# Performance work log

Hardware: AMD Instinct MI355X
Metric: run time of the kernel (lower is better)

## Reference

```python
import jax, jax.numpy as jnp
import numpy as np

H = 8
D_MODEL = 512
D_K = D_MODEL // H
NEG = -1e9


def setup_inputs() -> dict:
    key = jax.random.key(0)
    ks = jax.random.split(key, 12)
    N, Lq, Lk = 2, 4096, 4096
    inp = {
        "query": jax.random.normal(ks[0], (N, Lq, D_MODEL), dtype=jnp.float32),
        "key": jax.random.normal(ks[1], (N, Lk, D_MODEL), dtype=jnp.float32),
        "value": jax.random.normal(ks[2], (N, Lk, D_MODEL), dtype=jnp.float32),
        "mask": jnp.ones((N, 1, Lk), dtype=jnp.int32),
    }
    scale = 0.02
    for i, nm in enumerate(["q", "k", "v", "o"]):
        inp[f"W{nm}"] = scale * jax.random.normal(ks[3 + i], (D_MODEL, D_MODEL), dtype=jnp.float32)
        inp[f"b{nm}"] = jnp.zeros((D_MODEL,), dtype=jnp.float32)
    return inp


def reference(query, key, value, mask, Wq, bq, Wk, bk, Wv, bv, Wo, bo):
    # torch Linear: y = x @ W.T + b
    N, Lq, _ = query.shape
    Lk = key.shape[1]
    q = (query @ Wq.T + bq).reshape(N, Lq, H, D_K)   # (N,Lq,h,dk)
    k = (key @ Wk.T + bk).reshape(N, Lk, H, D_K)     # (N,Lk,h,dk)
    v = (value @ Wv.T + bv).reshape(N, Lk, H, D_K)   # (N,Lk,h,dk)
    # scores: (N,h,Lq,Lk)
    scores = jnp.einsum("bqhd,bkhd->bhqk", q, k) / jnp.sqrt(jnp.float32(D_K))
    # mask (N,1,Lk) or (N,Lq,Lk) -> broadcast over heads (and Lq if singleton)
    m = mask[:, None, :, :]  # (N,1,1|Lq,Lk)
    scores = jnp.where(m == 0, jnp.float32(NEG), scores)
    attn = jax.nn.softmax(scores, axis=-1)
    # dropout is identity in eval mode (deterministic reference)
    out = jnp.einsum("bhqk,bkhd->bqhd", attn, v).reshape(N, Lq, D_MODEL)
    return out @ Wo.T + bo
```

## Files before the change

### kernel.cpp

```cpp
#include <hip/hip_runtime.h>
#include <hip/hip_bf16.h>

#define H 8
#define DM 512
#define DK 64
#define LSEQ 4096
#define NB 2
#define NSPLIT 2
#define KSPAN (LSEQ / NSPLIT)
#define NIT (KSPAN / 64)

#define QSCALE 0.18033688011112042f

typedef float f32x4 __attribute__((ext_vector_type(4)));
typedef __bf16 bf16x8 __attribute__((ext_vector_type(8)));
typedef __bf16 bf16x2 __attribute__((ext_vector_type(2)));
typedef unsigned short u16;

__device__ __forceinline__ u16 f2bf(float f) {
    union { float f; unsigned u; } v{f};
    return (u16)((v.u + 0x8000u) >> 16);
}

__device__ __forceinline__ unsigned pkbf(float a, float b) {
#if __has_builtin(__builtin_amdgcn_cvt_pk_bf16_f32)
    union { bf16x2 v; unsigned u; } x;
    x.v = __builtin_amdgcn_cvt_pk_bf16_f32(a, b);
    return x.u;
#else
    union { float f; unsigned u; } x{a}, y{b};
    return ((x.u + 0x8000u) >> 16) | ((y.u + 0x8000u) & 0xffff0000u);
#endif
}

__device__ __forceinline__ ushort4 cvt4(float4 a) {
    union { ushort4 s; uint2 u; } o;
    o.u.x = pkbf(a.x, a.y);
    o.u.y = pkbf(a.z, a.w);
    return o.s;
}

__device__ __forceinline__ float2 ubf2(unsigned u) {
    union { float f; unsigned v; } a, b;
    a.v = u << 16;
    b.v = u & 0xffff0000u;
    return make_float2(a.f, b.f);
}

__device__ __forceinline__ float fexp2(float x) {
#if __has_builtin(__builtin_amdgcn_exp2f)
    return __builtin_amdgcn_exp2f(x);
#else
    return exp2f(x);
#endif
}

__device__ __forceinline__ f32x4 mfma32(bf16x8 a, bf16x8 b, f32x4 c) {
    return __builtin_amdgcn_mfma_f32_16x16x32_bf16(a, b, c, 0, 0, 0);
}

__launch_bounds__(256, 2)
__global__ void proj_qkv(const float* __restrict__ Xq, const float* __restrict__ Xk,
                         const float* __restrict__ Xv,
                         const float* __restrict__ Wq, const float* __restrict__ Wk,
                         const float* __restrict__ Wv,
                         const float* __restrict__ bq, const float* __restrict__ bk,
                         const float* __restrict__ bv,
                         const int* __restrict__ mask,
                         u16* __restrict__ qo, u16* __restrict__ ko, u16* __restrict__ vo)
{
    const int mode = blockIdx.z;
    const float* X    = (mode == 0) ? Xq : (mode == 1) ? Xk : Xv;
    const float* W    = (mode == 0) ? Wq : (mode == 1) ? Wk : Wv;
    const float* bias = (mode == 0) ? bq : (mode == 1) ? bk : bv;
    u16* out          = (mode == 0) ? qo : (mode == 1) ? ko : vo;

    __shared__ __align__(16) u16 As[2][128][72];
    __shared__ __align__(16) u16 Bs[2][128][72];

    const int tid  = threadIdx.x;
    const int wave = tid >> 6;
    const int lane = tid & 63;
    const int g    = lane >> 4;
    const int ln   = lane & 15;
    const int wr   = wave >> 1;
    const int wc   = wave & 1;

    const int m0 = blockIdx.x * 128;
    const int n0 = blockIdx.y * 128;

    float4 xa[8], wb[8];
    #pragma unroll
    for (int i = 0; i < 8; ++i) {
        int idx = tid + 256 * i;
        int row = idx >> 4;
        int col = (idx & 15) * 4;
        xa[i] = *(const float4*)(X + (size_t)(m0 + row) * DM + col);
        wb[i] = *(const float4*)(W + (size_t)(n0 + row) * DM + col);
    }
    #pragma unroll
    for (int i = 0; i < 8; ++i) {
        int idx = tid + 256 * i;
        int row = idx >> 4;
        int col = (idx & 15) * 4;
        *(ushort4*)&As[0][row][col] = cvt4(xa[i]);
        *(ushort4*)&Bs[0][row][col] = cvt4(wb[i]);
    }

    f32x4 acc[4][4] = {};

    for (int kt = 0; kt < 8; ++kt) {
        const int cur = kt & 1;
        __syncthreads();

        if (kt < 7) {
            int kb = (kt + 1) * 64;
            #pragma unroll
            for (int i = 0; i < 8; ++i) {
                int idx = tid + 256 * i;
                int row = idx >> 4;
                int col = (idx & 15) * 4;
                xa[i] = *(const float4*)(X + (size_t)(m0 + row) * DM + kb + col);
                wb[i] = *(const float4*)(W + (size_t)(n0 + row) * DM + kb + col);
            }
        }

        bf16x8 af[4][2], bf[4][2];
        #pragma unroll
        for (int t = 0; t < 4; ++t) {
            af[t][0] = *(const bf16x8*)&As[cur][wr * 64 + t * 16 + ln][g * 8];
            af[t][1] = *(const bf16x8*)&As[cur][wr * 64 + t * 16 + ln][32 + g * 8];
            bf[t][0] = *(const bf16x8*)&Bs[cur][wc * 64 + t * 16 + ln][g * 8];
            bf[t][1] = *(const bf16x8*)&Bs[cur][wc * 64 + t * 16 + ln][32 + g * 8];
        }
        #pragma unroll
        for (int mt = 0; mt < 4; ++mt)
            #pragma unroll
            for (int nt = 0; nt < 4; ++nt) {
                acc[mt][nt] = mfma32(af[mt][0], bf[nt][0], acc[mt][nt]);
                acc[mt][nt] = mfma32(af[mt][1], bf[nt][1], acc[mt][nt]);
            }

        if (kt < 7) {
            int nxt = 1 - cur;
            #pragma unroll
            for (int i = 0; i < 8; ++i) {
                int idx = tid + 256 * i;
                int row = idx >> 4;
                int col = (idx & 15) * 4;
                *(ushort4*)&As[nxt][row][col] = cvt4(xa[i]);
                *(ushort4*)&Bs[nxt][row][col] = cvt4(wb[i]);
            }
        }
    }

    if (mode != 2) {
        #pragma unroll
        for (int nt = 0; nt < 4; ++nt) {
            int n  = n0 + wc * 64 + nt * 16 + ln;
            float bias_n = bias[n];
            int hh = n >> 6;
            int d  = n & (DK - 1);
            #pragma unroll
            for (int mt = 0; mt < 4; ++mt)
                #pragma unroll
                for (int r = 0; r < 4; ++r) {
                    int m  = m0 + wr * 64 + mt * 16 + g * 4 + r;
                    int bb = m >> 12;
                    int s  = m & (LSEQ - 1);
                    float val = acc[mt][nt][r] + bias_n;
                    if (mode == 0) val *= QSCALE;
                    else           val = mask[bb * LSEQ + s] ? val : 0.0f;
                    out[(size_t)((bb * H + hh) * LSEQ + s) * DK + d] = f2bf(val);
                }
        }
    } else {
        __syncthreads();
        u16* Ts = &As[0][0][0];
        const int bb = m0 >> 12;
        const int s0 = m0 & (LSEQ - 1);
        #pragma unroll
        for (int nt = 0; nt < 4; ++nt) {
            int dl = wc * 64 + nt * 16 + ln;
            float bias_n = bias[n0 + dl];
            #pragma unroll
            for (int mt = 0; mt < 4; ++mt)
                #pragma unroll
                for (int r = 0; r < 4; ++r) {
                    int sl = wr * 64 + mt * 16 + g * 4 + r;
                    float val = acc[mt][nt][r] + bias_n;
                    val = mask[bb * LSEQ + s0 + sl] ? val : 0.0f;
                    Ts[dl * 136 + sl] = f2bf(val);
                }
        }
        __syncthreads();
        int dl   = tid >> 1;
        int half = tid & 1;
        int n  = n0 + dl;
        int hh = n >> 6;
        int d  = n & (DK - 1);
        int sb = s0 + half * 64;
        u16* dst = out + ((size_t)((bb * H + hh) * DK + d) * LSEQ + sb);
        const u16* srcp = Ts + dl * 136 + half * 64;
        #pragma unroll
        for (int i = 0; i < 8; ++i)
            *(uint4*)(dst + i * 8) = *(const uint4*)(srcp + i * 8);
    }
}

__launch_bounds__(256, 4)
__global__ void flash(const u16* __restrict__ qws, const u16* __restrict__ kws,
                      const u16* __restrict__ vws, const int* __restrict__ mask,
                      u16* __restrict__ Opart, float* __restrict__ lpart)
{
    __shared__ u16 Ks[2][64][72];
    __shared__ u16 Vs[2][64][72];

    const int tid   = threadIdx.x;
    const int wave  = tid >> 6;
    const int lane  = tid & 63;
    const int g     = lane >> 4;
    const int ln    = lane & 15;
    const int b     = blockIdx.z;
    const int h     = blockIdx.y;
    const int qblk  = blockIdx.x & 31;
    const int split = blockIdx.x >> 5;
    const int q0    = qblk * 128;
    const int kstart = split * KSPAN;

    const u16* qp = qws + ((size_t)((b * H + h) * LSEQ) + q0 + wave * 32 + ln) * DK;
    const u16* kp = kws + (size_t)(b * H + h) * LSEQ * DK;
    const u16* vp = vws + (size_t)(b * H + h) * DK * LSEQ;
    const int* mp = mask + b * LSEQ;

    int nmask = 0;
    for (int t = 0; t < NIT; ++t) {
        int mval = mp[kstart + t * 64 + lane];
        unsigned long long bal = __ballot(mval == 0);
        nmask += (int)__popcll(bal);
    }
    const float fnmask = (float)nmask;

    bf16x8 qf[2][2];
    qf[0][0] = *(const bf16x8*)(qp + g * 8);
    qf[0][1] = *(const bf16x8*)(qp + 32 + g * 8);
    qf[1][0] = *(const bf16x8*)(qp + 16 * DK + g * 8);
    qf[1][1] = *(const bf16x8*)(qp + 16 * DK + 32 + g * 8);

    union OU { unsigned u[4]; bf16x8 v; } onesu;
    onesu.u[0] = onesu.u[1] = onesu.u[2] = onesu.u[3] = 0x3F803F80u;
    const bf16x8 vones = onesu.v;

    f32x4 accO[2][4] = {};
    f32x4 accL[2] = {};

    const int row = tid >> 3;
    const int c   = tid & 7;
    const int vcol0 = ((2 * c) & 3) * 16 + (c >> 1) * 4;

    uint4 kr0, kr1, vr0, vr1;
    kr0 = *(const uint4*)(kp + (size_t)(kstart + row) * DK + c * 8);
    kr1 = *(const uint4*)(kp + (size_t)(kstart + row + 32) * DK + c * 8);
    vr0 = *(const uint4*)(vp + (size_t)row * LSEQ + kstart + c * 8);
    vr1 = *(const uint4*)(vp + (size_t)(row + 32) * LSEQ + kstart + c * 8);
    *(uint4*)&Ks[0][row][c * 8]      = kr0;
    *(uint4*)&Ks[0][row + 32][c * 8] = kr1;
    *(uint2*)&Vs[0][row][vcol0]           = make_uint2(vr0.x, vr0.y);
    *(uint2*)&Vs[0][row][vcol0 + 16]      = make_uint2(vr0.z, vr0.w);
    *(uint2*)&Vs[0][row + 32][vcol0]      = make_uint2(vr1.x, vr1.y);
    *(uint2*)&Vs[0][row + 32][vcol0 + 16] = make_uint2(vr1.z, vr1.w);

    for (int it = 0; it < NIT; ++it) {
        const int cur = it & 1;
        __syncthreads();

        if (it < NIT - 1) {
            int kn = kstart + it * 64 + 64;
            kr0 = *(const uint4*)(kp + (size_t)(kn + row) * DK + c * 8);
            kr1 = *(const uint4*)(kp + (size_t)(kn + row + 32) * DK + c * 8);
            vr0 = *(const uint4*)(vp + (size_t)row * LSEQ + kn + c * 8);
            vr1 = *(const uint4*)(vp + (size_t)(row + 32) * LSEQ + kn + c * 8);
        }

        f32x4 sc[2][4];
        #pragma unroll
        for (int kb = 0; kb < 4; ++kb) {
            bf16x8 kf0 = *(const bf16x8*)&Ks[cur][kb * 16 + ln][g * 8];
            bf16x8 kf1 = *(const bf16x8*)&Ks[cur][kb * 16 + ln][32 + g * 8];
            #pragma unroll
            for (int j = 0; j < 2; ++j) {
                f32x4 z = {};
                z = mfma32(kf0, qf[j][0], z);
                z = mfma32(kf1, qf[j][1], z);
                sc[j][kb] = z;
            }
        }

        #pragma unroll
        for (int kb = 0; kb < 4; ++kb)
            #pragma unroll
            for (int j = 0; j < 2; ++j) {
                sc[j][kb][0] = fexp2(sc[j][kb][0]);
                sc[j][kb][1] = fexp2(sc[j][kb][1]);
                sc[j][kb][2] = fexp2(sc[j][kb][2]);
                sc[j][kb][3] = fexp2(sc[j][kb][3]);
            }

        union PU { unsigned u[4]; bf16x8 v; } p01[2], p23[2];
        #pragma unroll
        for (int j = 0; j < 2; ++j) {
            p01[j].u[0] = pkbf(sc[j][0][0], sc[j][0][1]);
            p01[j].u[1] = pkbf(sc[j][0][2], sc[j][0][3]);
            p01[j].u[2] = pkbf(sc[j][1][0], sc[j][1][1]);
            p01[j].u[3] = pkbf(sc[j][1][2], sc[j][1][3]);
            p23[j].u[0] = pkbf(sc[j][2][0], sc[j][2][1]);
            p23[j].u[1] = pkbf(sc[j][2][2], sc[j][2][3]);
            p23[j].u[2] = pkbf(sc[j][3][0], sc[j][3][1]);
            p23[j].u[3] = pkbf(sc[j][3][2], sc[j][3][3]);
        }

        #pragma unroll
        for (int j = 0; j < 2; ++j) {
            accL[j] = mfma32(p01[j].v, vones, accL[j]);
            accL[j] = mfma32(p23[j].v, vones, accL[j]);
        }
        #pragma unroll
        for (int t = 0; t < 4; ++t) {
            bf16x8 vb01 = *(const bf16x8*)&Vs[cur][t * 16 + ln][g * 16];
            bf16x8 vb23 = *(const bf16x8*)&Vs[cur][t * 16 + ln][g * 16 + 8];
            #pragma unroll
            for (int j = 0; j < 2; ++j) {
                accO[j][t] = mfma32(p01[j].v, vb01, accO[j][t]);
                accO[j][t] = mfma32(p23[j].v, vb23, accO[j][t]);
            }
        }

        if (it < NIT - 1) {
            int nxt = 1 - cur;
            *(uint4*)&Ks[nxt][row][c * 8]      = kr0;
            *(uint4*)&Ks[nxt][row + 32][c * 8] = kr1;
            *(uint2*)&Vs[nxt][row][vcol0]           = make_uint2(vr0.x, vr0.y);
            *(uint2*)&Vs[nxt][row][vcol0 + 16]      = make_uint2(vr0.z, vr0.w);
            *(uint2*)&Vs[nxt][row + 32][vcol0]      = make_uint2(vr1.x, vr1.y);
            *(uint2*)&Vs[nxt][row + 32][vcol0 + 16] = make_uint2(vr1.z, vr1.w);
        }
    }

    const size_t PLANE = (size_t)NB * LSEQ * DM;
    u16* opp = Opart + (size_t)split * PLANE;

    #pragma unroll
    for (int j = 0; j < 2; ++j) {
        if (ln == 0) {
            #pragma unroll
            for (int r = 0; r < 4; ++r)
                lpart[(size_t)split * (NB * H * LSEQ) + ((size_t)(b * H + h) * LSEQ)
                      + q0 + wave * 32 + j * 16 + g * 4 + r] = accL[j][r] - fnmask;
        }
        #pragma unroll
        for (int r = 0; r < 4; ++r) {
            float linv = 1.0f / (accL[j][r] - fnmask);
            size_t base = ((size_t)(b * LSEQ) + q0 + wave * 32 + j * 16 + g * 4 + r) * DM + h * DK;
            #pragma unroll
            for (int t = 0; t < 4; ++t)
                opp[base + t * 16 + ln] = f2bf(accO[j][t][r] * linv);
        }
    }
}

__launch_bounds__(256, 4)
__global__ void reduce_split(const u16* __restrict__ Opart, const float* __restrict__ lpart,
                             u16* __restrict__ ows)
{
    const size_t PLANE = (size_t)NB * LSEQ * DM;
    size_t gid  = (size_t)blockIdx.x * 256 + threadIdx.x;
    size_t flat = gid * 8;

    int b   = (int)(flat >> 21);
    int rem = (int)(flat & ((1 << 21) - 1));
    int q   = rem >> 9;
    int hh  = (rem & 511) >> 6;
    size_t lidx = ((size_t)(b * H + hh) * LSEQ) + q;

    float l0 = lpart[lidx];
    float l1 = lpart[(size_t)NB * H * LSEQ + lidx];
    float inv = 1.0f / (l0 + l1);
    float w0 = l0 * inv, w1 = l1 * inv;

    uint4 c0 = *(const uint4*)(Opart + flat);
    uint4 c1 = *(const uint4*)(Opart + PLANE + flat);

    float o[8];
    {
        float2 a, bv;
        a = ubf2(c0.x); bv = ubf2(c1.x); o[0] = w0 * a.x + w1 * bv.x; o[1] = w0 * a.y + w1 * bv.y;
        a = ubf2(c0.y); bv = ubf2(c1.y); o[2] = w0 * a.x + w1 * bv.x; o[3] = w0 * a.y + w1 * bv.y;
        a = ubf2(c0.z); bv = ubf2(c1.z); o[4] = w0 * a.x + w1 * bv.x; o[5] = w0 * a.y + w1 * bv.y;
        a = ubf2(c0.w); bv = ubf2(c1.w); o[6] = w0 * a.x + w1 * bv.x; o[7] = w0 * a.y + w1 * bv.y;
    }
    uint4 r;
    r.x = pkbf(o[0], o[1]);
    r.y = pkbf(o[2], o[3]);
    r.z = pkbf(o[4], o[5]);
    r.w = pkbf(o[6], o[7]);
    *(uint4*)(ows + flat) = r;
}

__launch_bounds__(256, 2)
__global__ void proj_out(const u16* __restrict__ A, const float* __restrict__ Wo,
                         const float* __restrict__ bo, float* __restrict__ out)
{
    __shared__ __align__(16) u16 As[2][128][72];
    __shared__ __align__(16) u16 Bs[2][64][72];

    const int tid  = threadIdx.x;
    const int wave = tid >> 6;
    const int lane = tid & 63;
    const int g    = lane >> 4;
    const int ln   = lane & 15;

    const int m0 = blockIdx.x * 128;
    const int n0 = blockIdx.y * 64;

    uint4 aa[4];
    float4 wb[4];
    #pragma unroll
    for (int i = 0; i < 4; ++i) {
        int idx = tid + 256 * i;
        int row = idx >> 3;
        int col = (idx & 7) * 8;
        aa[i] = *(const uint4*)(A + (size_t)(m0 + row) * DM + col);
        int rwb = idx >> 4;
        int cwb = (idx & 15) * 4;
        wb[i] = *(const float4*)(Wo + (size_t)(n0 + rwb) * DM + cwb);
    }
    #pragma unroll
    for (int i = 0; i < 4; ++i) {
        int idx = tid + 256 * i;
        int row = idx >> 3;
        int col = (idx & 7) * 8;
        *(uint4*)&As[0][row][col] = aa[i];
        int rwb = idx >> 4;
        int cwb = (idx & 15) * 4;
        *(ushort4*)&Bs[0][rwb][cwb] = cvt4(wb[i]);
    }

    f32x4 acc[2][4] = {};

    for (int kt = 0; kt < 8; ++kt) {
        const int cur = kt & 1;
        __syncthreads();

        if (kt < 7) {
            int kb = (kt + 1) * 64;
            #pragma unroll
            for (int i = 0; i < 4; ++i) {
                int idx = tid + 256 * i;
                int row = idx >> 3;
                int col = (idx & 7) * 8;
                aa[i] = *(const uint4*)(A + (size_t)(m0 + row) * DM + kb + col);
                int rwb = idx >> 4;
                int cwb = (idx & 15) * 4;
                wb[i] = *(const float4*)(Wo + (size_t)(n0 + rwb) * DM + kb + cwb);
            }
        }

        bf16x8 af[2][2], bf[4][2];
        #pragma unroll
        for (int mt = 0; mt < 2; ++mt) {
            af[mt][0] = *(const bf16x8*)&As[cur][wave * 32 + mt * 16 + ln][g * 8];
            af[mt][1] = *(const bf16x8*)&As[cur][wave * 32 + mt * 16 + ln][32 + g * 8];
        }
        #pragma unroll
        for (int nt = 0; nt < 4; ++nt) {
            bf[nt][0] = *(const bf16x8*)&Bs[cur][nt * 16 + ln][g * 8];
            bf[nt][1] = *(const bf16x8*)&Bs[cur][nt * 16 + ln][32 + g * 8];
        }
        #pragma unroll
        for (int mt = 0; mt < 2; ++mt)
            #pragma unroll
            for (int nt = 0; nt < 4; ++nt) {
                acc[mt][nt] = mfma32(af[mt][0], bf[nt][0], acc[mt][nt]);
                acc[mt][nt] = mfma32(af[mt][1], bf[nt][1], acc[mt][nt]);
            }

        if (kt < 7) {
            int nxt = 1 - cur;
            #pragma unroll
            for (int i = 0; i < 4; ++i) {
                int idx = tid + 256 * i;
                int row = idx >> 3;
                int col = (idx & 7) * 8;
                *(uint4*)&As[nxt][row][col] = aa[i];
                int rwb = idx >> 4;
                int cwb = (idx & 15) * 4;
                *(ushort4*)&Bs[nxt][rwb][cwb] = cvt4(wb[i]);
            }
        }
    }

    #pragma unroll
    for (int nt = 0; nt < 4; ++nt) {
        int n = n0 + nt * 16 + ln;
        float bias_n = bo[n];
        #pragma unroll
        for (int mt = 0; mt < 2; ++mt)
            #pragma unroll
            for (int r = 0; r < 4; ++r) {
                int m = m0 + wave * 32 + mt * 16 + g * 4 + r;
                out[(size_t)m * DM + n] = acc[mt][nt][r] + bias_n;
            }
    }
}

extern "C" void kernel_launch(void* const* d_in, const int* in_sizes, int n_in,
                              void* d_out, int out_size, void* d_ws, size_t ws_size,
                              hipStream_t stream) {
    (void)in_sizes; (void)n_in; (void)out_size; (void)ws_size;

    const float* query = (const float*)d_in[0];
    const float* key   = (const float*)d_in[1];
    const float* value = (const float*)d_in[2];
    const int*   mask  = (const int*)d_in[3];
    const float* Wq = (const float*)d_in[4];
    const float* bq = (const float*)d_in[5];
    const float* Wk = (const float*)d_in[6];
    const float* bk = (const float*)d_in[7];
    const float* Wv = (const float*)d_in[8];
    const float* bv = (const float*)d_in[9];
    const float* Wo = (const float*)d_in[10];
    const float* bo = (const float*)d_in[11];
    float* out = (float*)d_out;

    const size_t PLANE = (size_t)NB * H * LSEQ * DK;
    u16* qws   = (u16*)d_ws;
    u16* kws   = qws + PLANE;
    u16* vws   = kws + PLANE;
    u16* ows   = vws + PLANE;
    u16* Opart = ows + PLANE;
    float* lpart = (float*)(Opart + (size_t)NSPLIT * PLANE);

    dim3 blk(256);
    proj_qkv<<<dim3(64, 4, 3), blk, 0, stream>>>(query, key, value, Wq, Wk, Wv,
                                                 bq, bk, bv, mask, qws, kws, vws);
    flash<<<dim3(32 * NSPLIT, H, NB), blk, 0, stream>>>(qws, kws, vws, mask, Opart, lpart);
    reduce_split<<<dim3(2048), blk, 0, stream>>>(Opart, lpart, ows);
    proj_out<<<dim3(64, 8, 1), blk, 0, stream>>>(ows, Wo, bo, out);
}
```

Measured before the change: 231.3 us.

## Swizzle flash attention LDS tiles, add MFMA priority hints, raise occupancy bounds

Replaces the padded K/V shared-memory tiles in the flash kernel with unpadded 64-wide tiles using an XOR swizzle on 8-element chunks. This shrinks LDS use while aiming to avoid bank conflicts on the fragment reads. It also wraps the MFMA sections in s_setprio hints, raises launch-bounds occupancy for flash and proj_out, and reduces proj_out padding from 72 to 68. A padding of 68 may break 16-byte alignment for uint4 accesses, and the higher occupancy targets may force register spills.

```diff
diff --git a/kernel.cpp b/kernel.cpp
--- a/kernel.cpp
+++ b/kernel.cpp
@@ -208,13 +208,13 @@
     }
 }
 
-__launch_bounds__(256, 4)
+__launch_bounds__(256, 5)
 __global__ void flash(const u16* __restrict__ qws, const u16* __restrict__ kws,
                       const u16* __restrict__ vws, const int* __restrict__ mask,
                       u16* __restrict__ Opart, float* __restrict__ lpart)
 {
-    __shared__ u16 Ks[2][64][72];
-    __shared__ u16 Vs[2][64][72];
+    __shared__ u16 Ks[2][64][64];
+    __shared__ u16 Vs[2][64][64];
 
     const int tid   = threadIdx.x;
     const int wave  = tid >> 6;
@@ -256,19 +256,26 @@
 
     const int row = tid >> 3;
     const int c   = tid & 7;
+    const int swz = row & 7;
+    const int kcol = (c ^ swz) * 8;
     const int vcol0 = ((2 * c) & 3) * 16 + (c >> 1) * 4;
+    const int vs0 = vcol0 >> 3;
+    const int vof = vcol0 & 7;
+    const int vw0 = ((vs0 ^ swz) * 8) + vof;
+    const int vw1 = (((vs0 + 2) ^ swz) * 8) + vof;
+    const int rs = ln & 7;
 
     uint4 kr0, kr1, vr0, vr1;
     kr0 = *(const uint4*)(kp + (size_t)(kstart + row) * DK + c * 8);
     kr1 = *(const uint4*)(kp + (size_t)(kstart + row + 32) * DK + c * 8);
     vr0 = *(const uint4*)(vp + (size_t)row * LSEQ + kstart + c * 8);
     vr1 = *(const uint4*)(vp + (size_t)(row + 32) * LSEQ + kstart + c * 8);
-    *(uint4*)&Ks[0][row][c * 8]      = kr0;
-    *(uint4*)&Ks[0][row + 32][c * 8] = kr1;
-    *(uint2*)&Vs[0][row][vcol0]           = make_uint2(vr0.x, vr0.y);
-    *(uint2*)&Vs[0][row][vcol0 + 16]      = make_uint2(vr0.z, vr0.w);
-    *(uint2*)&Vs[0][row + 32][vcol0]      = make_uint2(vr1.x, vr1.y);
-    *(uint2*)&Vs[0][row + 32][vcol0 + 16] = make_uint2(vr1.z, vr1.w);
+    *(uint4*)&Ks[0][row][kcol]      = kr0;
+    *(uint4*)&Ks[0][row + 32][kcol] = kr1;
+    *(uint2*)&Vs[0][row][vw0]       = make_uint2(vr0.x, vr0.y);
+    *(uint2*)&Vs[0][row][vw1]       = make_uint2(vr0.z, vr0.w);
+    *(uint2*)&Vs[0][row + 32][vw0]  = make_uint2(vr1.x, vr1.y);
+    *(uint2*)&Vs[0][row + 32][vw1]  = make_uint2(vr1.z, vr1.w);
 
     for (int it = 0; it < NIT; ++it) {
         const int cur = it & 1;
@@ -282,11 +289,12 @@
             vr1 = *(const uint4*)(vp + (size_t)(row + 32) * LSEQ + kn + c * 8);
         }
 
+        __builtin_amdgcn_s_setprio(1);
         f32x4 sc[2][4];
         #pragma unroll
         for (int kb = 0; kb < 4; ++kb) {
-            bf16x8 kf0 = *(const bf16x8*)&Ks[cur][kb * 16 + ln][g * 8];
-            bf16x8 kf1 = *(const bf16x8*)&Ks[cur][kb * 16 + ln][32 + g * 8];
+            bf16x8 kf0 = *(const bf16x8*)&Ks[cur][kb * 16 + ln][(g ^ rs) * 8];
+            bf16x8 kf1 = *(const bf16x8*)&Ks[cur][kb * 16 + ln][((g + 4) ^ rs) * 8];
             #pragma unroll
             for (int j = 0; j < 2; ++j) {
                 f32x4 z = {};
@@ -295,6 +303,7 @@
                 sc[j][kb] = z;
             }
         }
+        __builtin_amdgcn_s_setprio(0);
 
         #pragma unroll
         for (int kb = 0; kb < 4; ++kb)
@@ -319,6 +328,7 @@
             p23[j].u[3] = pkbf(sc[j][3][2], sc[j][3][3]);
         }
 
+        __builtin_amdgcn_s_setprio(1);
         #pragma unroll
         for (int j = 0; j < 2; ++j) {
             accL[j] = mfma32(p01[j].v, vones, accL[j]);
@@ -326,23 +336,24 @@
         }
         #pragma unroll
         for (int t = 0; t < 4; ++t) {
-            bf16x8 vb01 = *(const bf16x8*)&Vs[cur][t * 16 + ln][g * 16];
-            bf16x8 vb23 = *(const bf16x8*)&Vs[cur][t * 16 + ln][g * 16 + 8];
+            bf16x8 vb01 = *(const bf16x8*)&Vs[cur][t * 16 + ln][((2 * g) ^ rs) * 8];
+            bf16x8 vb23 = *(const bf16x8*)&Vs[cur][t * 16 + ln][((2 * g + 1) ^ rs) * 8];
             #pragma unroll
             for (int j = 0; j < 2; ++j) {
                 accO[j][t] = mfma32(p01[j].v, vb01, accO[j][t]);
                 accO[j][t] = mfma32(p23[j].v, vb23, accO[j][t]);
             }
         }
+        __builtin_amdgcn_s_setprio(0);
 
         if (it < NIT - 1) {
             int nxt = 1 - cur;
-            *(uint4*)&Ks[nxt][row][c * 8]      = kr0;
-            *(uint4*)&Ks[nxt][row + 32][c * 8] = kr1;
-            *(uint2*)&Vs[nxt][row][vcol0]           = make_uint2(vr0.x, vr0.y);
-            *(uint2*)&Vs[nxt][row][vcol0 + 16]      = make_uint2(vr0.z, vr0.w);
-            *(uint2*)&Vs[nxt][row + 32][vcol0]      = make_uint2(vr1.x, vr1.y);
-            *(uint2*)&Vs[nxt][row + 32][vcol0 + 16] = make_uint2(vr1.z, vr1.w);
+            *(uint4*)&Ks[nxt][row][kcol]      = kr0;
+            *(uint4*)&Ks[nxt][row + 32][kcol] = kr1;
+            *(uint2*)&Vs[nxt][row][vw0]       = make_uint2(vr0.x, vr0.y);
+            *(uint2*)&Vs[nxt][row][vw1]       = make_uint2(vr0.z, vr0.w);
+            *(uint2*)&Vs[nxt][row + 32][vw0]  = make_uint2(vr1.x, vr1.y);
+            *(uint2*)&Vs[nxt][row + 32][vw1]  = make_uint2(vr1.z, vr1.w);
         }
     }
 
@@ -406,12 +417,12 @@
     *(uint4*)(ows + flat) = r;
 }
 
-__launch_bounds__(256, 2)
+__launch_bounds__(256, 3)
 __global__ void proj_out(const u16* __restrict__ A, const float* __restrict__ Wo,
                          const float* __restrict__ bo, float* __restrict__ out)
 {
-    __shared__ __align__(16) u16 As[2][128][72];
-    __shared__ __align__(16) u16 Bs[2][64][72];
+    __shared__ __align__(16) u16 As[2][128][68];
+    __shared__ __align__(16) u16 Bs[2][64][68];
 
     const int tid  = threadIdx.x;
     const int wave = tid >> 6;
```

Result: slower. 436.0 us (+88.5%).
